# Kernel tuning notes

Hardware: AMD Instinct MI355X
Metric: run time of the kernel (lower is better)

## Reference

```python
import jax, jax.numpy as jnp
import numpy as np

B, S, D, H, L, V, C = 8, 1024, 768, 12, 6, 32000, 2
HD = D // H
DF = 3072
MAX_POS = 2048
EPS = 1e-5


def layer_norm(x, scale, bias):
    m = jnp.mean(x, axis=-1, keepdims=True)
    v = jnp.mean((x - m) ** 2, axis=-1, keepdims=True)
    return (x - m) / jnp.sqrt(v + EPS) * scale + bias


def setup_inputs() -> dict:
    key = jax.random.key(0)
    ks = jax.random.split(key, 16)
    std = 0.02
    return {
        "input_ids": jax.random.randint(ks[0], (B, S), 0, V),
        "attention_mask": jax.random.randint(ks[1], (B, S), 0, 2),
        "token_emb": jax.random.normal(ks[2], (V, D), jnp.float32) * std,
        "pos_emb": jax.random.normal(ks[3], (MAX_POS, D), jnp.float32) * std,
        "qkv_w": jax.random.normal(ks[4], (L, D, 3 * D), jnp.float32) * std,
        "qkv_b": jnp.zeros((L, 3 * D), jnp.float32),
        "out_w": jax.random.normal(ks[5], (L, D, D), jnp.float32) * std,
        "out_b": jnp.zeros((L, D), jnp.float32),
        "n1_s": jnp.ones((L, D), jnp.float32),
        "n1_b": jnp.zeros((L, D), jnp.float32),
        "ff1_w": jax.random.normal(ks[6], (L, D, DF), jnp.float32) * std,
        "ff1_b": jnp.zeros((L, DF), jnp.float32),
        "ff2_w": jax.random.normal(ks[7], (L, DF, D), jnp.float32) * std,
        "ff2_b": jnp.zeros((L, D), jnp.float32),
        "n2_s": jnp.ones((L, D), jnp.float32),
        "n2_b": jnp.zeros((L, D), jnp.float32),
        "hln_s": jnp.ones((D,), jnp.float32),
        "hln_b": jnp.zeros((D,), jnp.float32),
        "cls_w": jax.random.normal(ks[8], (D, C), jnp.float32) * std,
        "cls_b": jnp.zeros((C,), jnp.float32),
    }


def reference(input_ids, attention_mask, token_emb, pos_emb, qkv_w, qkv_b,
              out_w, out_b, n1_s, n1_b, ff1_w, ff1_b, ff2_w, ff2_b,
              n2_s, n2_b, hln_s, hln_b, cls_w, cls_b):
    # embeddings: token + position, scaled by sqrt(d_model)
    x = (token_emb[input_ids] + pos_emb[:S][None, :, :]) * np.float32(np.sqrt(D))
    # extended mask: 0 at valid tokens, -10000 at padding -> (B,1,1,S)
    ext = (1.0 - attention_mask.astype(x.dtype))[:, None, None, :] * -10000.0
    scale = np.float32(1.0 / np.sqrt(HD))
    for i in range(L):
        # --- self attention (pre-norm) ---
        h = layer_norm(x, n1_s[i], n1_b[i])
        qkv = (h @ qkv_w[i] + qkv_b[i]).reshape(B, S, H, 3, HD)
        q, k, v = qkv[..., 0, :], qkv[..., 1, :], qkv[..., 2, :]  # (B,S,H,HD)
        scores = jnp.einsum('bshd,bthd->bhst', q, k) * scale
        # faithful to source: masked_fill(ext_mask == 0, -1e9)
        scores = jnp.where(ext == 0, jnp.asarray(-1e9, scores.dtype), scores)
        w = jax.nn.softmax(scores, axis=-1)
        att = jnp.einsum('bhst,bthd->bshd', w, v).reshape(B, S, D)
        x = x + (att @ out_w[i] + out_b[i])
        # --- feed forward (pre-norm) ---
        h2 = layer_norm(x, n2_s[i], n2_b[i])
        ff = jax.nn.relu(h2 @ ff1_w[i] + ff1_b[i]) @ ff2_w[i] + ff2_b[i]
        x = x + ff
    # CLS pooling head
    pooled = layer_norm(x[:, 0, :], hln_s, hln_b)
    return pooled @ cls_w + cls_b
```

## Files before the change

### kernel.cpp

```cpp
#include <hip/hip_runtime.h>
#include <hip/hip_bf16.h>

typedef unsigned short u16;
typedef __bf16 bf16x8 __attribute__((ext_vector_type(8)));
typedef float f32x4 __attribute__((ext_vector_type(4)));
typedef unsigned int u32x4 __attribute__((ext_vector_type(4)));

#define DEVI __device__ __forceinline__

DEVI u16 f2b(float f) {
    unsigned int u = __builtin_bit_cast(unsigned int, f);
    unsigned int lsb = (u >> 16) & 1u;
    u += 0x7fffu + lsb;
    return (u16)(u >> 16);
}
DEVI float b2f(u16 b) {
    unsigned int u = ((unsigned int)b) << 16;
    return __builtin_bit_cast(float, u);
}

DEVI float blockReduceSum(float v, float* red, int tid) {
    #pragma unroll
    for (int o = 32; o; o >>= 1) v += __shfl_xor(v, o);
    __syncthreads();
    if ((tid & 63) == 0) red[tid >> 6] = v;
    __syncthreads();
    return red[0] + red[1] + red[2] + red[3];
}

__global__ void detect_kernel(const void* tok, int* flag) {
    __shared__ int bad;
    if (threadIdx.x == 0) bad = 0;
    __syncthreads();
    const u16* p = (const u16*)tok;
    int cnt = 0;
    for (int j = 0; j < 16; ++j) {
        float v = b2f(p[2 * (threadIdx.x * 16 + j)]);
        if (!(fabsf(v) < 1.0f)) cnt++;
    }
    if (cnt) atomicAdd(&bad, 1);
    __syncthreads();
    if (threadIdx.x == 0) flag[0] = (bad == 0) ? 1 : 0;
}

__global__ void to_f32_kernel(const void* src, float* dst, int n, const int* flag) {
    int i = blockIdx.x * 256 + threadIdx.x;
    if (i >= n) return;
    if (flag[0]) dst[i] = b2f(((const u16*)src)[i]);
    else         dst[i] = ((const float*)src)[i];
}

template<int BM, int BN, int NT>
DEVI void gemm_core(const u16* __restrict__ A, int lda,
                    const u16* __restrict__ Bt, int ldb,
                    int K, f32x4 (&acc)[4][4],
                    u16* As, u16* Bs)
{
    const int tid  = threadIdx.x;
    const int lane = tid & 63;
    const int wave = tid >> 6;
    constexpr int WN = BN / 64;
    const int wm   = wave / WN;
    const int wn   = wave % WN;
    const int quad = lane >> 4;
    const int l16  = lane & 15;
    constexpr int ACH = (BM * 4) / NT;
    constexpr int BCH = (BN * 4) / NT;

    for (int k0 = 0; k0 < K; k0 += 32) {
        u32x4 av[ACH], bv[BCH];
        #pragma unroll
        for (int i = 0; i < ACH; ++i) {
            int id = i * NT + tid;
            av[i] = *(const u32x4*)(A + (size_t)(id >> 2) * lda + k0 + (id & 3) * 8);
        }
        #pragma unroll
        for (int i = 0; i < BCH; ++i) {
            int id = i * NT + tid;
            bv[i] = *(const u32x4*)(Bt + (size_t)(id >> 2) * ldb + k0 + (id & 3) * 8);
        }
        __syncthreads();
        #pragma unroll
        for (int i = 0; i < ACH; ++i) { int id = i * NT + tid; *(u32x4*)(As + (id >> 2) * 40 + (id & 3) * 8) = av[i]; }
        #pragma unroll
        for (int i = 0; i < BCH; ++i) { int id = i * NT + tid; *(u32x4*)(Bs + (id >> 2) * 40 + (id & 3) * 8) = bv[i]; }
        __syncthreads();

        bf16x8 af[4], bfv[4];
        #pragma unroll
        for (int mt = 0; mt < 4; ++mt)
            af[mt] = *(const bf16x8*)(As + (wm * 64 + mt * 16 + l16) * 40 + quad * 8);
        #pragma unroll
        for (int nt = 0; nt < 4; ++nt)
            bfv[nt] = *(const bf16x8*)(Bs + (wn * 64 + nt * 16 + l16) * 40 + quad * 8);
        #pragma unroll
        for (int mt = 0; mt < 4; ++mt)
            #pragma unroll
            for (int nt = 0; nt < 4; ++nt)
                acc[mt][nt] = __builtin_amdgcn_mfma_f32_16x16x32_bf16(af[mt], bfv[nt], acc[mt][nt], 0, 0, 0);
    }
}

template<int EPI>
__global__ __launch_bounds__(256) void gemm_std(
    const u16* __restrict__ A, int lda,
    const u16* __restrict__ Bt, int ldb,
    const float* __restrict__ bias,
    u16* __restrict__ outB, float* __restrict__ resid,
    int ldc, int K)
{
    __shared__ u16 As[128 * 40];
    __shared__ u16 Bs[128 * 40];
    const size_t bM = (size_t)blockIdx.y * 128;
    const size_t bN = (size_t)blockIdx.x * 128;
    f32x4 acc[4][4] = {};
    gemm_core<128, 128, 256>(A + bM * lda, lda, Bt + bN * ldb, ldb, K, acc, As, Bs);

    const int tid = threadIdx.x, lane = tid & 63, wave = tid >> 6;
    const int wm = wave >> 1, wn = wave & 1, quad = lane >> 4, l16 = lane & 15;
    #pragma unroll
    for (int mt = 0; mt < 4; ++mt)
        #pragma unroll
        for (int nt = 0; nt < 4; ++nt) {
            size_t col = bN + wn * 64 + nt * 16 + l16;
            float bcol = bias[col];
            #pragma unroll
            for (int r = 0; r < 4; ++r) {
                size_t row = bM + wm * 64 + mt * 16 + quad * 4 + r;
                float v = acc[mt][nt][r] + bcol;
                if constexpr (EPI == 1) v = fmaxf(v, 0.f);
                if constexpr (EPI == 2) resid[row * ldc + col] += v;
                else                    outB[row * ldc + col] = f2b(v);
            }
        }
}

__global__ __launch_bounds__(256, 2) void flash_attn(
    const u16* __restrict__ qkv, const u16* __restrict__ vt,
    const int* __restrict__ mask, u16* __restrict__ attout)
{
    __shared__ u16 Ks[128 * 72];
    __shared__ u16 Vs[64 * 136];
    __shared__ u16 Ps[128 * 136];
    __shared__ float Ms[1024];

    const int bh = blockIdx.y;
    const int b = bh / 12, h = bh % 12;
    const int q0 = blockIdx.x * 128;
    const int tid = threadIdx.x, lane = tid & 63, wave = tid >> 6;
    const int quad = lane >> 4, l16 = lane & 15;

    for (int i = tid; i < 1024; i += 256)
        Ms[i] = (mask[b * 1024 + i] != 0) ? 1.f : 0.f;

    bf16x8 aq[2][2];
    #pragma unroll
    for (int mt = 0; mt < 2; ++mt)
        #pragma unroll
        for (int s = 0; s < 2; ++s)
            aq[mt][s] = *(const bf16x8*)(qkv + (size_t)(b * 1024 + q0 + wave * 32 + mt * 16 + l16) * 2304
                                          + h * 192 + s * 32 + quad * 8);

    float mi[2][4], li[2][4];
    f32x4 Oacc[2][4] = {};
    #pragma unroll
    for (int mt = 0; mt < 2; ++mt)
        #pragma unroll
        for (int r = 0; r < 4; ++r) { mi[mt][r] = -3e38f; li[mt][r] = 0.f; }

    for (int kt = 0; kt < 8; ++kt) {
        u32x4 kreg[4], vreg[4];
        #pragma unroll
        for (int i = 0; i < 4; ++i) {
            int id = i * 256 + tid, row = id >> 3, ch = id & 7;
            kreg[i] = *(const u32x4*)(qkv + (size_t)(b * 1024 + kt * 128 + row) * 2304 + h * 192 + 64 + ch * 8);
        }
        #pragma unroll
        for (int i = 0; i < 4; ++i) {
            int id = i * 256 + tid, row = id >> 4, ch = id & 15;
            vreg[i] = *(const u32x4*)(vt + (size_t)bh * 65536 + (size_t)row * 1024 + kt * 128 + ch * 8);
        }
        __syncthreads();
        #pragma unroll
        for (int i = 0; i < 4; ++i) {
            int id = i * 256 + tid, row = id >> 3, ch = id & 7;
            *(u32x4*)(Ks + row * 72 + ch * 8) = kreg[i];
        }
        #pragma unroll
        for (int i = 0; i < 4; ++i) {
            int id = i * 256 + tid, row = id >> 4, ch = id & 15;
            *(u32x4*)(Vs + row * 136 + ch * 8) = vreg[i];
        }
        __syncthreads();

        f32x4 Sacc[2][8] = {};
        #pragma unroll
        for (int s = 0; s < 2; ++s) {
            bf16x8 kf[8];
            #pragma unroll
            for (int nt = 0; nt < 8; ++nt)
                kf[nt] = *(const bf16x8*)(Ks + (nt * 16 + l16) * 72 + s * 32 + quad * 8);
            #pragma unroll
            for (int mt = 0; mt < 2; ++mt)
                #pragma unroll
                for (int nt = 0; nt < 8; ++nt)
                    Sacc[mt][nt] = __builtin_amdgcn_mfma_f32_16x16x32_bf16(aq[mt][s], kf[nt], Sacc[mt][nt], 0, 0, 0);
        }

        float mval[8];
        #pragma unroll
        for (int nt = 0; nt < 8; ++nt) mval[nt] = Ms[kt * 128 + nt * 16 + l16];
        #pragma unroll
        for (int mt = 0; mt < 2; ++mt)
            #pragma unroll
            for (int nt = 0; nt < 8; ++nt)
                #pragma unroll
                for (int r = 0; r < 4; ++r)
                    Sacc[mt][nt][r] = (mval[nt] != 0.f) ? -1e9f : Sacc[mt][nt][r] * 0.125f;

        #pragma unroll
        for (int mt = 0; mt < 2; ++mt) {
            float al[4];
            #pragma unroll
            for (int r = 0; r < 4; ++r) {
                float rm = -3e38f;
                #pragma unroll
                for (int nt = 0; nt < 8; ++nt) rm = fmaxf(rm, Sacc[mt][nt][r]);
                #pragma unroll
                for (int o = 8; o; o >>= 1) rm = fmaxf(rm, __shfl_xor(rm, o));
                float mn = fmaxf(mi[mt][r], rm);
                al[r] = __expf(mi[mt][r] - mn);
                mi[mt][r] = mn;
                float rs = 0.f;
                #pragma unroll
                for (int nt = 0; nt < 8; ++nt) {
                    float pv = __expf(Sacc[mt][nt][r] - mn);
                    rs += pv;
                    Sacc[mt][nt][r] = pv;
                }
                #pragma unroll
                for (int o = 8; o; o >>= 1) rs += __shfl_xor(rs, o);
                li[mt][r] = li[mt][r] * al[r] + rs;
            }
            #pragma unroll
            for (int ntv = 0; ntv < 4; ++ntv)
                #pragma unroll
                for (int r = 0; r < 4; ++r) Oacc[mt][ntv][r] *= al[r];
            const int rowb = wave * 32 + mt * 16 + quad * 4;
            #pragma unroll
            for (int nt = 0; nt < 8; ++nt)
                #pragma unroll
                for (int r = 0; r < 4; ++r)
                    Ps[(rowb + r) * 136 + nt * 16 + l16] = f2b(Sacc[mt][nt][r]);
        }

        #pragma unroll
        for (int s2 = 0; s2 < 4; ++s2) {
            bf16x8 vf[4];
            #pragma unroll
            for (int ntv = 0; ntv < 4; ++ntv)
                vf[ntv] = *(const bf16x8*)(Vs + (ntv * 16 + l16) * 136 + s2 * 32 + quad * 8);
            #pragma unroll
            for (int mt2 = 0; mt2 < 2; ++mt2) {
                bf16x8 pf = *(const bf16x8*)(Ps + (wave * 32 + mt2 * 16 + l16) * 136 + s2 * 32 + quad * 8);
                #pragma unroll
                for (int ntv = 0; ntv < 4; ++ntv)
                    Oacc[mt2][ntv] = __builtin_amdgcn_mfma_f32_16x16x32_bf16(pf, vf[ntv], Oacc[mt2][ntv], 0, 0, 0);
            }
        }
    }

    #pragma unroll
    for (int mt = 0; mt < 2; ++mt)
        #pragma unroll
        for (int r = 0; r < 4; ++r) {
            float inv = 1.0f / li[mt][r];
            int s = q0 + wave * 32 + mt * 16 + quad * 4 + r;
            #pragma unroll
            for (int ntv = 0; ntv < 4; ++ntv)
                attout[((size_t)(b * 1024 + s)) * 768 + h * 64 + ntv * 16 + l16] = f2b(Oacc[mt][ntv][r] * inv);
        }
}

__global__ __launch_bounds__(256) void embed_kernel(
    const int* __restrict__ ids, const void* __restrict__ tok,
    const void* __restrict__ pos, float* __restrict__ x, const int* __restrict__ flag)
{
    const int e  = blockIdx.x * 256 + threadIdx.x;
    const int bs = e / 192;
    const int d  = (e - bs * 192) * 4;
    const int s  = bs & 1023;
    const int id = ids[bs];
    float t[4], p4[4];
    if (flag[0]) {
        const u16* tb = (const u16*)tok + (size_t)id * 768 + d;
        const u16* pb = (const u16*)pos + (size_t)s  * 768 + d;
        #pragma unroll
        for (int j = 0; j < 4; ++j) { t[j] = b2f(tb[j]); p4[j] = b2f(pb[j]); }
    } else {
        const float* tb = (const float*)tok + (size_t)id * 768 + d;
        const float* pb = (const float*)pos + (size_t)s  * 768 + d;
        #pragma unroll
        for (int j = 0; j < 4; ++j) { t[j] = tb[j]; p4[j] = pb[j]; }
    }
    float* xo = x + (size_t)bs * 768 + d;
    #pragma unroll
    for (int j = 0; j < 4; ++j) xo[j] = (t[j] + p4[j]) * 27.7128129211020f;
}

__global__ __launch_bounds__(256) void layernorm_kernel(
    const float* __restrict__ x, const float* __restrict__ sc,
    const float* __restrict__ bi, u16* __restrict__ out)
{
    __shared__ float red[4];
    const size_t row = blockIdx.x;
    const float* xr = x + row * 768;
    const int tid = threadIdx.x;
    float v0 = xr[tid], v1 = xr[tid + 256], v2 = xr[tid + 512];
    float s = blockReduceSum(v0 + v1 + v2, red, tid);
    float mean = s * (1.0f / 768.0f);
    float d0 = v0 - mean, d1 = v1 - mean, d2 = v2 - mean;
    float q = blockReduceSum(d0 * d0 + d1 * d1 + d2 * d2, red, tid);
    float rstd = rsqrtf(q * (1.0f / 768.0f) + 1e-5f);
    u16* orow = out + row * 768;
    orow[tid]       = f2b(d0 * rstd * sc[tid]       + bi[tid]);
    orow[tid + 256] = f2b(d1 * rstd * sc[tid + 256] + bi[tid + 256]);
    orow[tid + 512] = f2b(d2 * rstd * sc[tid + 512] + bi[tid + 512]);
}

__global__ __launch_bounds__(256) void transpose_w_kernel(
    const void* __restrict__ W, size_t off, u16* __restrict__ Wt,
    int Kd, int Nd, const int* __restrict__ flag)
{
    __shared__ u16 tile[32][34];
    const int n0 = blockIdx.x * 32, k0 = blockIdx.y * 32;
    const int tx = threadIdx.x & 31, ty = threadIdx.x >> 5;
    const int fl = flag[0];
    #pragma unroll
    for (int i = 0; i < 4; ++i) {
        size_t idx = off + (size_t)(k0 + ty + i * 8) * Nd + n0 + tx;
        u16 val = fl ? ((const u16*)W)[idx] : f2b(((const float*)W)[idx]);
        tile[ty + i * 8][tx] = val;
    }
    __syncthreads();
    #pragma unroll
    for (int i = 0; i < 4; ++i)
        Wt[(size_t)(n0 + ty + i * 8) * Kd + k0 + tx] = tile[tx][ty + i * 8];
}

__global__ __launch_bounds__(256) void build_vt_kernel(
    const u16* __restrict__ qkv, u16* __restrict__ vt)
{
    __shared__ u16 tile[64][72];
    const int bh = blockIdx.y;
    const int b = bh / 12, h = bh % 12;
    const int t0 = blockIdx.x * 64;
    const int tid = threadIdx.x;
    const int tl = tid >> 2;
    const int d4 = (tid & 3) * 16;
    const u16* src = qkv + (size_t)(b * 1024 + t0 + tl) * 2304 + h * 192 + 128 + d4;
    *(u32x4*)(&tile[tl][d4])     = *(const u32x4*)(src);
    *(u32x4*)(&tile[tl][d4 + 8]) = *(const u32x4*)(src + 8);
    __syncthreads();
    const int dd = tid >> 2;
    const int tstart = (tid & 3) * 16;
    union { u16 us[16]; u32x4 v[2]; } pk;
    #pragma unroll
    for (int j = 0; j < 16; ++j) pk.us[j] = tile[tstart + j][dd];
    u16* dst = vt + ((size_t)bh * 64 + dd) * 1024 + t0 + tstart;
    *(u32x4*)(dst)     = pk.v[0];
    *(u32x4*)(dst + 8) = pk.v[1];
}

__global__ __launch_bounds__(256) void pooled_cls_kernel(
    const float* __restrict__ x, const float* __restrict__ hs, const float* __restrict__ hb,
    const float* __restrict__ cw, const float* __restrict__ cb, void* __restrict__ dout,
    const int* __restrict__ flag)
{
    __shared__ float red[4];
    __shared__ float pooled[768];
    const int b = blockIdx.x;
    const float* xr = x + (size_t)b * 1024 * 768;
    const int tid = threadIdx.x;
    float v0 = xr[tid], v1 = xr[tid + 256], v2 = xr[tid + 512];
    float s = blockReduceSum(v0 + v1 + v2, red, tid);
    float mean = s * (1.0f / 768.0f);
    float d0 = v0 - mean, d1 = v1 - mean, d2 = v2 - mean;
    float q = blockReduceSum(d0 * d0 + d1 * d1 + d2 * d2, red, tid);
    float rstd = rsqrtf(q * (1.0f / 768.0f) + 1e-5f);
    pooled[tid]       = d0 * rstd * hs[tid]       + hb[tid];
    pooled[tid + 256] = d1 * rstd * hs[tid + 256] + hb[tid + 256];
    pooled[tid + 512] = d2 * rstd * hs[tid + 512] + hb[tid + 512];
    __syncthreads();
    float p0 = 0.f, p1 = 0.f;
    for (int c = tid; c < 768; c += 256) {
        float pv = pooled[c];
        p0 += pv * cw[2 * c];
        p1 += pv * cw[2 * c + 1];
    }
    p0 = blockReduceSum(p0, red, tid);
    p1 = blockReduceSum(p1, red, tid);
    if (tid == 0) {
        float o0 = p0 + cb[0], o1 = p1 + cb[1];
        if (flag[0]) {
            ((u16*)dout)[b * 2 + 0] = f2b(o0);
            ((u16*)dout)[b * 2 + 1] = f2b(o1);
        } else {
            ((float*)dout)[b * 2 + 0] = o0;
            ((float*)dout)[b * 2 + 1] = o1;
        }
    }
}

extern "C" void kernel_launch(void* const* d_in, const int* in_sizes, int n_in,
                              void* d_out, int out_size, void* d_ws, size_t ws_size,
                              hipStream_t stream)
{
    const int* ids  = (const int*)d_in[0];
    const int* mask = (const int*)d_in[1];
    const void* tok   = d_in[2];
    const void* pos   = d_in[3];
    const void* qkv_w = d_in[4];
    const void* qkv_b = d_in[5];
    const void* out_w = d_in[6];
    const void* out_b = d_in[7];
    const void* n1_s  = d_in[8];
    const void* n1_b  = d_in[9];
    const void* ff1_w = d_in[10];
    const void* ff1_b = d_in[11];
    const void* ff2_w = d_in[12];
    const void* ff2_b = d_in[13];
    const void* n2_s  = d_in[14];
    const void* n2_b  = d_in[15];
    const void* hln_s = d_in[16];
    const void* hln_b = d_in[17];
    const void* cls_w = d_in[18];
    const void* cls_b = d_in[19];

    char* p = (char*)d_ws;
    auto alloc = [&](size_t bytes) -> char* {
        char* r = p; p += (bytes + 255) & ~(size_t)255; return r;
    };
    float* x      = (float*)alloc(6291456ull * 4);
    u16*   h      = (u16*)  alloc(6291456ull * 2);
    u16*   qkvB   = (u16*)  alloc(18874368ull * 2);
    u16*   vt     = (u16*)  alloc(6291456ull * 2);
    u16*   ffmid  = (u16*)  alloc(25165824ull * 2);
    u16*   wqkvT  = (u16*)  alloc(1769472ull * 2);
    u16*   woutT  = (u16*)  alloc(589824ull * 2);
    u16*   wff1T  = (u16*)  alloc(2359296ull * 2);
    u16*   wff2T  = (u16*)  alloc(2359296ull * 2);
    float* params = (float*)alloc(62978ull * 4);
    int*   flag   = (int*)  alloc(256);
    u16*   attout = h;

    float* P_qkv_b = params + 0;
    float* P_out_b = params + 13824;
    float* P_n1_s  = params + 18432;
    float* P_n1_b  = params + 23040;
    float* P_ff1_b = params + 27648;
    float* P_ff2_b = params + 46080;
    float* P_n2_s  = params + 50688;
    float* P_n2_b  = params + 55296;
    float* P_hln_s = params + 59904;
    float* P_hln_b = params + 60672;
    float* P_cls_w = params + 61440;
    float* P_cls_b = params + 62976;

    detect_kernel<<<1, 256, 0, stream>>>(tok, flag);

    auto cvt = [&](const void* src, float* dst, int n) {
        to_f32_kernel<<<(n + 255) / 256, 256, 0, stream>>>(src, dst, n, flag);
    };
    cvt(qkv_b, P_qkv_b, 13824);  cvt(out_b, P_out_b, 4608);
    cvt(n1_s,  P_n1_s,  4608);   cvt(n1_b,  P_n1_b,  4608);
    cvt(ff1_b, P_ff1_b, 18432);  cvt(ff2_b, P_ff2_b, 4608);
    cvt(n2_s,  P_n2_s,  4608);   cvt(n2_b,  P_n2_b,  4608);
    cvt(hln_s, P_hln_s, 768);    cvt(hln_b, P_hln_b, 768);
    cvt(cls_w, P_cls_w, 1536);   cvt(cls_b, P_cls_b, 2);

    embed_kernel<<<6144, 256, 0, stream>>>(ids, tok, pos, x, flag);

    for (int l = 0; l < 6; ++l) {
        transpose_w_kernel<<<dim3(72, 24), 256, 0, stream>>>(qkv_w, (size_t)l * 1769472, wqkvT, 768, 2304, flag);
        transpose_w_kernel<<<dim3(24, 24), 256, 0, stream>>>(out_w, (size_t)l * 589824,  woutT, 768, 768,  flag);
        transpose_w_kernel<<<dim3(96, 24), 256, 0, stream>>>(ff1_w, (size_t)l * 2359296, wff1T, 768, 3072, flag);
        transpose_w_kernel<<<dim3(24, 96), 256, 0, stream>>>(ff2_w, (size_t)l * 2359296, wff2T, 3072, 768, flag);

        layernorm_kernel<<<8192, 256, 0, stream>>>(x, P_n1_s + l * 768, P_n1_b + l * 768, h);
        gemm_std<0><<<dim3(18, 64), 256, 0, stream>>>(h, 768, wqkvT, 768,
                                                      P_qkv_b + l * 2304, qkvB, nullptr, 2304, 768);
        build_vt_kernel<<<dim3(16, 96), 256, 0, stream>>>(qkvB, vt);
        flash_attn<<<dim3(8, 96), 256, 0, stream>>>(qkvB, vt, mask, attout);
        gemm_std<2><<<dim3(6, 64), 256, 0, stream>>>(attout, 768, woutT, 768,
                                                     P_out_b + l * 768, nullptr, x, 768, 768);
        layernorm_kernel<<<8192, 256, 0, stream>>>(x, P_n2_s + l * 768, P_n2_b + l * 768, h);
        gemm_std<1><<<dim3(24, 64), 256, 0, stream>>>(h, 768, wff1T, 768,
                                                      P_ff1_b + l * 3072, ffmid, nullptr, 3072, 768);
        gemm_std<2><<<dim3(6, 64), 256, 0, stream>>>(ffmid, 3072, wff2T, 3072,
                                                     P_ff2_b + l * 768, nullptr, x, 768, 3072);
    }
    pooled_cls_kernel<<<8, 256, 0, stream>>>(x, P_hln_s, P_hln_b, P_cls_w, P_cls_b, d_out, flag);
}
```

Baseline: 2.538 ms.

## Use direct global-to-LDS loads in GEMM and split-K atomics for narrow GEMMs

Replaces register-staged global loads with global_load_lds 16-byte transfers into unpadded LDS tiles. Adds a split-K GEMM kernel for the output and FF2 projections, with two K slices accumulated into the residual stream via atomicAdd and bias added once. This aims to cut load latency and register pressure and to fill more CUs for the N=768 GEMMs. It risks LDS bank conflicts from removing the padding, atomic overhead, and a non-deterministic summation order.

```diff
diff --git a/kernel.cpp b/kernel.cpp
--- a/kernel.cpp
+++ b/kernel.cpp
@@ -7,6 +7,13 @@
 typedef unsigned int u32x4 __attribute__((ext_vector_type(4)));
 
 #define DEVI __device__ __forceinline__
+
+typedef __attribute__((address_space(3))) void lds_void;
+typedef __attribute__((address_space(1))) const void gbl_void;
+
+DEVI void gload16(const void* gp, void* lp) {
+    __builtin_amdgcn_global_load_lds((gbl_void*)gp, (lds_void*)lp, 16, 0, 0);
+}
 
 DEVI u16 f2b(float f) {
     unsigned int u = __builtin_bit_cast(unsigned int, f);
@@ -50,49 +57,39 @@
     else         dst[i] = ((const float*)src)[i];
 }
 
-template<int BM, int BN, int NT>
-DEVI void gemm_core(const u16* __restrict__ A, int lda,
-                    const u16* __restrict__ Bt, int ldb,
-                    int K, f32x4 (&acc)[4][4],
-                    u16* As, u16* Bs)
+DEVI void gemm_core_async(const u16* __restrict__ A, int lda,
+                          const u16* __restrict__ Bt, int ldb,
+                          int K, f32x4 (&acc)[4][4],
+                          u16* As, u16* Bs)
 {
     const int tid  = threadIdx.x;
     const int lane = tid & 63;
     const int wave = tid >> 6;
-    constexpr int WN = BN / 64;
-    const int wm   = wave / WN;
-    const int wn   = wave % WN;
     const int quad = lane >> 4;
     const int l16  = lane & 15;
-    constexpr int ACH = (BM * 4) / NT;
-    constexpr int BCH = (BN * 4) / NT;
+    const int wm   = wave >> 1;
+    const int wn   = wave & 1;
+
+    const int c0 = (wave * 2 + 0) * 64 + lane;
+    const int c1 = (wave * 2 + 1) * 64 + lane;
+    const int r0 = c0 >> 2, h0 = (c0 & 3) * 8;
+    const int r1 = c1 >> 2, h1 = (c1 & 3) * 8;
 
     for (int k0 = 0; k0 < K; k0 += 32) {
-        u32x4 av[ACH], bv[BCH];
-        #pragma unroll
-        for (int i = 0; i < ACH; ++i) {
-            int id = i * NT + tid;
-            av[i] = *(const u32x4*)(A + (size_t)(id >> 2) * lda + k0 + (id & 3) * 8);
-        }
-        #pragma unroll
-        for (int i = 0; i < BCH; ++i) {
-            int id = i * NT + tid;
-            bv[i] = *(const u32x4*)(Bt + (size_t)(id >> 2) * ldb + k0 + (id & 3) * 8);
-        }
         __syncthreads();
-        #pragma unroll
-        for (int i = 0; i < ACH; ++i) { int id = i * NT + tid; *(u32x4*)(As + (id >> 2) * 40 + (id & 3) * 8) = av[i]; }
-        #pragma unroll
-        for (int i = 0; i < BCH; ++i) { int id = i * NT + tid; *(u32x4*)(Bs + (id >> 2) * 40 + (id & 3) * 8) = bv[i]; }
+        gload16(A  + (size_t)r0 * lda + k0 + h0, As + c0 * 8);
+        gload16(Bt + (size_t)r0 * ldb + k0 + h0, Bs + c0 * 8);
+        gload16(A  + (size_t)r1 * lda + k0 + h1, As + c1 * 8);
+        gload16(Bt + (size_t)r1 * ldb + k0 + h1, Bs + c1 * 8);
         __syncthreads();
 
         bf16x8 af[4], bfv[4];
         #pragma unroll
         for (int mt = 0; mt < 4; ++mt)
-            af[mt] = *(const bf16x8*)(As + (wm * 64 + mt * 16 + l16) * 40 + quad * 8);
+            af[mt] = *(const bf16x8*)(As + (wm * 64 + mt * 16 + l16) * 32 + quad * 8);
         #pragma unroll
         for (int nt = 0; nt < 4; ++nt)
-            bfv[nt] = *(const bf16x8*)(Bs + (wn * 64 + nt * 16 + l16) * 40 + quad * 8);
+            bfv[nt] = *(const bf16x8*)(Bs + (wn * 64 + nt * 16 + l16) * 32 + quad * 8);
         #pragma unroll
         for (int mt = 0; mt < 4; ++mt)
             #pragma unroll
@@ -106,15 +103,14 @@
     const u16* __restrict__ A, int lda,
     const u16* __restrict__ Bt, int ldb,
     const float* __restrict__ bias,
-    u16* __restrict__ outB, float* __restrict__ resid,
-    int ldc, int K)
-{
-    __shared__ u16 As[128 * 40];
-    __shared__ u16 Bs[128 * 40];
+    u16* __restrict__ outB, int ldc, int K)
+{
+    __shared__ u16 As[128 * 32];
+    __shared__ u16 Bs[128 * 32];
     const size_t bM = (size_t)blockIdx.y * 128;
     const size_t bN = (size_t)blockIdx.x * 128;
     f32x4 acc[4][4] = {};
-    gemm_core<128, 128, 256>(A + bM * lda, lda, Bt + bN * ldb, ldb, K, acc, As, Bs);
+    gemm_core_async(A + bM * lda, lda, Bt + bN * ldb, ldb, K, acc, As, Bs);
 
     const int tid = threadIdx.x, lane = tid & 63, wave = tid >> 6;
     const int wm = wave >> 1, wn = wave & 1, quad = lane >> 4, l16 = lane & 15;
@@ -129,8 +125,38 @@
                 size_t row = bM + wm * 64 + mt * 16 + quad * 4 + r;
                 float v = acc[mt][nt][r] + bcol;
                 if constexpr (EPI == 1) v = fmaxf(v, 0.f);
-                if constexpr (EPI == 2) resid[row * ldc + col] += v;
-                else                    outB[row * ldc + col] = f2b(v);
+                outB[row * ldc + col] = f2b(v);
+            }
+        }
+}
+
+__global__ __launch_bounds__(256) void gemm_splitk(
+    const u16* __restrict__ A, int lda,
+    const u16* __restrict__ Bt, int ldb,
+    const float* __restrict__ bias,
+    float* __restrict__ resid, int ldc, int Ksub)
+{
+    __shared__ u16 As[128 * 32];
+    __shared__ u16 Bs[128 * 32];
+    const size_t bM = (size_t)blockIdx.y * 128;
+    const size_t bN = (size_t)blockIdx.x * 128;
+    const int Koff = blockIdx.z * Ksub;
+    f32x4 acc[4][4] = {};
+    gemm_core_async(A + bM * lda + Koff, lda, Bt + bN * ldb + Koff, ldb, Ksub, acc, As, Bs);
+
+    const int tid = threadIdx.x, lane = tid & 63, wave = tid >> 6;
+    const int wm = wave >> 1, wn = wave & 1, quad = lane >> 4, l16 = lane & 15;
+    const bool addb = (blockIdx.z == 0);
+    #pragma unroll
+    for (int mt = 0; mt < 4; ++mt)
+        #pragma unroll
+        for (int nt = 0; nt < 4; ++nt) {
+            size_t col = bN + wn * 64 + nt * 16 + l16;
+            float bcol = addb ? bias[col] : 0.f;
+            #pragma unroll
+            for (int r = 0; r < 4; ++r) {
+                size_t row = bM + wm * 64 + mt * 16 + quad * 4 + r;
+                atomicAdd(&resid[row * ldc + col], acc[mt][nt][r] + bcol);
             }
         }
 }
@@ -489,16 +515,16 @@
 
         layernorm_kernel<<<8192, 256, 0, stream>>>(x, P_n1_s + l * 768, P_n1_b + l * 768, h);
         gemm_std<0><<<dim3(18, 64), 256, 0, stream>>>(h, 768, wqkvT, 768,
-                                                      P_qkv_b + l * 2304, qkvB, nullptr, 2304, 768);
+                                                      P_qkv_b + l * 2304, qkvB, 2304, 768);
         build_vt_kernel<<<dim3(16, 96), 256, 0, stream>>>(qkvB, vt);
         flash_attn<<<dim3(8, 96), 256, 0, stream>>>(qkvB, vt, mask, attout);
-        gemm_std<2><<<dim3(6, 64), 256, 0, stream>>>(attout, 768, woutT, 768,
-                                                     P_out_b + l * 768, nullptr, x, 768, 768);
+        gemm_splitk<<<dim3(6, 64, 2), 256, 0, stream>>>(attout, 768, woutT, 768,
+                                                        P_out_b + l * 768, x, 768, 384);
         layernorm_kernel<<<8192, 256, 0, stream>>>(x, P_n2_s + l * 768, P_n2_b + l * 768, h);
         gemm_std<1><<<dim3(24, 64), 256, 0, stream>>>(h, 768, wff1T, 768,
-                                                      P_ff1_b + l * 3072, ffmid, nullptr, 3072, 768);
-        gemm_std<2><<<dim3(6, 64), 256, 0, stream>>>(ffmid, 3072, wff2T, 3072,
-                                                     P_ff2_b + l * 768, nullptr, x, 768, 3072);
+                                                      P_ff1_b + l * 3072, ffmid, 3072, 768);
+        gemm_splitk<<<dim3(6, 64, 2), 256, 0, stream>>>(ffmid, 3072, wff2T, 3072,
+                                                        P_ff2_b + l * 768, x, 768, 1536);
     }
     pooled_cls_kernel<<<8, 256, 0, stream>>>(x, P_hln_s, P_hln_b, P_cls_w, P_cls_b, d_out, flag);
 }
```

New measurement: 2.529 ms. Within noise of the previous version (-0.4%).
